# Performance work log

Hardware: AMD Instinct MI355X
Metric: run time of the kernel (lower is better)

The kernel has to match this reference:

```python
import jax, jax.numpy as jnp
import numpy as np

BIAS_BOUND = 8.0

def setup_inputs() -> dict:
    key = jax.random.key(0)
    k1, k2, k3 = jax.random.split(key, 3)
    x = jax.random.normal(k1, (8192, 4096), dtype=jnp.float32)
    # original init: uniform(-1.5, 1.5) for weight, uniform(-bias_bound, bias_bound) for bias
    weight = jax.random.uniform(k2, (4096, 4096), dtype=jnp.float32, minval=-1.5, maxval=1.5)
    bias = jax.random.uniform(k3, (4096,), dtype=jnp.float32, minval=-BIAS_BOUND, maxval=BIAS_BOUND)
    return {"x": x, "weight": weight, "bias": bias}

def reference(x, weight, bias):
    # temperature = 0 path: hard ternary quantization of weights
    w = jnp.clip(jnp.sign(jnp.round(weight)), -1.0, 1.0)      # [out, in] in {-1,0,1}
    b = jnp.clip(jnp.round(bias), -BIAS_BOUND, BIAS_BOUND)    # integer-valued bias
    # F.linear: x @ w.T + b
    return jnp.einsum('ni,oi->no', x, w) + b
```

## Files before the change

kernel.cpp:

```cpp
#include <hip/hip_runtime.h>
#include <hip/hip_bf16.h>
#include <stdint.h>

typedef __bf16 bf16x8 __attribute__((ext_vector_type(8)));
typedef float f32x4 __attribute__((ext_vector_type(4)));

#define AS1 __attribute__((address_space(1)))
#define AS3 __attribute__((address_space(3)))

__global__ void cvt_kernel(const float* __restrict__ x, const float* __restrict__ w,
                           __bf16* __restrict__ xb, __bf16* __restrict__ wb,
                           size_t nx8, size_t ntot8) {
    size_t i = (size_t)blockIdx.x * blockDim.x + threadIdx.x;
    size_t stride = (size_t)gridDim.x * blockDim.x;
    for (; i < ntot8; i += stride) {
        if (i < nx8) {
            size_t base = i * 8;
            float4 f0 = *reinterpret_cast<const float4*>(x + base);
            float4 f1 = *reinterpret_cast<const float4*>(x + base + 4);
            bf16x8 o;
            o[0] = (__bf16)f0.x; o[1] = (__bf16)f0.y; o[2] = (__bf16)f0.z; o[3] = (__bf16)f0.w;
            o[4] = (__bf16)f1.x; o[5] = (__bf16)f1.y; o[6] = (__bf16)f1.z; o[7] = (__bf16)f1.w;
            *reinterpret_cast<bf16x8*>(xb + base) = o;
        } else {
            size_t base = (i - nx8) * 8;
            float4 f0 = *reinterpret_cast<const float4*>(w + base);
            float4 f1 = *reinterpret_cast<const float4*>(w + base + 4);
            float f[8] = {f0.x, f0.y, f0.z, f0.w, f1.x, f1.y, f1.z, f1.w};
            bf16x8 o;
#pragma unroll
            for (int j = 0; j < 8; ++j) {
                float tv = (f[j] > 0.5f) ? 1.0f : ((f[j] < -0.5f) ? -1.0f : 0.0f);
                o[j] = (__bf16)tv;
            }
            *reinterpret_cast<bf16x8*>(wb + base) = o;
        }
    }
}


#define GLOAD(srcp, dstoff) \
    __builtin_amdgcn_global_load_lds((const AS1 void*)(srcp), \
        (AS3 void*)(lds + (dstoff)), 16, 0, 0)

#define STAGE_A0(DB, KT) do { GLOAD(srcA00 + (size_t)(KT)*64, (DB)*65536 +     0 + t*16); \
                              GLOAD(srcA01 + (size_t)(KT)*64, (DB)*65536 +  8192 + t*16); } while(0)
#define STAGE_A1(DB, KT) do { GLOAD(srcA10 + (size_t)(KT)*64, (DB)*65536 + 16384 + t*16); \
                              GLOAD(srcA11 + (size_t)(KT)*64, (DB)*65536 + 24576 + t*16); } while(0)
#define STAGE_B0(DB, KT) do { GLOAD(srcB00 + (size_t)(KT)*64, (DB)*65536 + 32768 + t*16); \
                              GLOAD(srcB01 + (size_t)(KT)*64, (DB)*65536 + 40960 + t*16); } while(0)
#define STAGE_B1(DB, KT) do { GLOAD(srcB10 + (size_t)(KT)*64, (DB)*65536 + 49152 + t*16); \
                              GLOAD(srcB11 + (size_t)(KT)*64, (DB)*65536 + 57344 + t*16); } while(0)

#define LD8(off) (*(const bf16x8*)(lds + (off)))

#define PHASE_SYNC_PRE() do { asm volatile("" ::: "memory"); \
    __builtin_amdgcn_s_barrier(); \
    asm volatile("s_waitcnt lgkmcnt(0)" ::: "memory"); \
    __builtin_amdgcn_sched_barrier(0); } while(0)

#define PHASE_SYNC_POST() do { __builtin_amdgcn_sched_barrier(0); \
    asm volatile("" ::: "memory"); \
    __builtin_amdgcn_s_barrier(); \
    asm volatile("" ::: "memory"); } while(0)

#define MFMA_QUAD(I0, J0) do { \
    __builtin_amdgcn_s_setprio(1); \
    _Pragma("unroll") for (int kk2 = 0; kk2 < 2; ++kk2) \
    _Pragma("unroll") for (int ii2 = 0; ii2 < 4; ++ii2) \
    _Pragma("unroll") for (int jj2 = 0; jj2 < 2; ++jj2) \
        acc[(I0)+ii2][(J0)+jj2] = __builtin_amdgcn_mfma_f32_16x16x32_bf16( \
            af[ii2][kk2], bfr[(J0)+jj2][kk2], acc[(I0)+ii2][(J0)+jj2], 0, 0, 0); \
    __builtin_amdgcn_s_setprio(0); } while(0)

__global__ __launch_bounds__(512, 2) void gemm_kernel(
    const __bf16* __restrict__ A, const __bf16* __restrict__ B,
    const float* __restrict__ bias, float* __restrict__ out,
    int M, int N, int K) {
    __shared__ __align__(16) unsigned char lds[131072];

    const int t    = threadIdx.x;
    const int lane = t & 63;
    const int wave = t >> 6;
    const int wm   = wave >> 2;
    const int wn   = wave & 3;
    const int fr   = lane & 15;
    const int kg   = lane >> 4;
    const int NT   = K >> 6;

    const int nwg  = gridDim.x * gridDim.y;
    int flat = blockIdx.y * gridDim.x + blockIdx.x;
    if ((nwg & 7) == 0) {
        const int cpx = nwg >> 3;
        flat = (flat & 7) * cpx + (flat >> 3);
    }
    const int blockCol = (flat % gridDim.x) * 256;
    const int blockRow = (flat / gridDim.x) * 256;

    const int tq  = t >> 3;
    const int gce = ((t & 7) ^ (tq & 7)) * 8;
    const __bf16* srcA00 = A + (size_t)(blockRow +   0 + tq) * K + gce;
    const __bf16* srcA01 = A + (size_t)(blockRow + 128 + tq) * K + gce;
    const __bf16* srcA10 = A + (size_t)(blockRow +  64 + tq) * K + gce;
    const __bf16* srcA11 = A + (size_t)(blockRow + 192 + tq) * K + gce;
    const int brB = (tq >> 5) * 64 + (tq & 31);
    const __bf16* srcB00 = B + (size_t)(blockCol +       brB) * K + gce;
    const __bf16* srcB01 = B + (size_t)(blockCol + 128 + brB) * K + gce;
    const __bf16* srcB10 = B + (size_t)(blockCol +  32 + brB) * K + gce;
    const __bf16* srcB11 = B + (size_t)(blockCol + 128 + 32 + brB) * K + gce;

    int offA[8], offB[4];
#pragma unroll
    for (int i = 0; i < 8; ++i)
        offA[i] = (((i >> 2) * 128 + wm * 64 + (i & 3) * 16 + fr) << 7);
#pragma unroll
    for (int j = 0; j < 4; ++j)
        offB[j] = 32768 + ((((j >> 1) * 128 + wn * 32 + (j & 1) * 16 + fr)) << 7);
    const int sw0 = ((kg ^ (fr & 7)) << 4);
    const int sw1 = sw0 ^ 64;

    f32x4 acc[8][4] = {};
    bf16x8 af[4][2];
    bf16x8 bfr[4][2];

    STAGE_A0(0, 0); STAGE_A1(0, 0); STAGE_B0(0, 0); STAGE_B1(0, 0);
    if (NT > 1) { STAGE_B0(1, 1); STAGE_A0(1, 1); STAGE_B1(1, 1); }
    if (NT > 1) { asm volatile("s_waitcnt vmcnt(6)" ::: "memory"); }
    else        { asm volatile("s_waitcnt vmcnt(0)" ::: "memory"); }
    __builtin_amdgcn_s_barrier();
    asm volatile("" ::: "memory");

    for (int kt = 0; kt < NT; ++kt) {
        const int db  = kt & 1;
        const int dbB = db << 16;
        const bool pf1 = (kt + 1 < NT);
        const bool pf2 = (kt + 2 < NT);

#pragma unroll
        for (int ii = 0; ii < 4; ++ii) {
            af[ii][0] = LD8(dbB + offA[ii] + sw0);
            af[ii][1] = LD8(dbB + offA[ii] + sw1);
        }
#pragma unroll
        for (int jj = 0; jj < 2; ++jj) {
            bfr[jj][0] = LD8(dbB + offB[jj] + sw0);
            bfr[jj][1] = LD8(dbB + offB[jj] + sw1);
        }
        if (pf1) STAGE_A1(db ^ 1, kt + 1);
        PHASE_SYNC_PRE();
        MFMA_QUAD(0, 0);
        PHASE_SYNC_POST();

#pragma unroll
        for (int jj = 2; jj < 4; ++jj) {
            bfr[jj][0] = LD8(dbB + offB[jj] + sw0);
            bfr[jj][1] = LD8(dbB + offB[jj] + sw1);
        }
        if (pf2) STAGE_B0(db, kt + 2);
        PHASE_SYNC_PRE();
        MFMA_QUAD(0, 2);
        PHASE_SYNC_POST();

#pragma unroll
        for (int ii = 0; ii < 4; ++ii) {
            af[ii][0] = LD8(dbB + offA[ii + 4] + sw0);
            af[ii][1] = LD8(dbB + offA[ii + 4] + sw1);
        }
        if (pf2) STAGE_A0(db, kt + 2);
        PHASE_SYNC_PRE();
        MFMA_QUAD(4, 2);
        PHASE_SYNC_POST();

        if (pf2) STAGE_B1(db, kt + 2);
        if (pf2)      { asm volatile("s_waitcnt vmcnt(6)" ::: "memory"); }
        else if (pf1) { asm volatile("s_waitcnt vmcnt(0)" ::: "memory"); }
        PHASE_SYNC_PRE();
        MFMA_QUAD(4, 0);
        PHASE_SYNC_POST();
    }

#pragma unroll
    for (int j = 0; j < 4; ++j) {
        const int col = blockCol + wn * 64 + j * 16 + fr;
        const float bq = fminf(8.0f, fmaxf(-8.0f, rintf(bias[col])));
#pragma unroll
        for (int i = 0; i < 8; ++i) {
            const int row0 = blockRow + wm * 128 + i * 16 + kg * 4;
#pragma unroll
            for (int r = 0; r < 4; ++r)
                out[(size_t)(row0 + r) * N + col] = acc[i][j][r] + bq;
        }
    }
}

__global__ void naive_kernel(const float* __restrict__ X, const float* __restrict__ W,
                             const float* __restrict__ bias, float* __restrict__ out,
                             int M, int N, int K) {
    int n = blockIdx.x * 16 + (threadIdx.x & 15);
    int m = blockIdx.y * 16 + (threadIdx.x >> 4);
    if (m >= M || n >= N) return;
    float acc = 0.f;
    for (int k = 0; k < K; ++k) {
        float w = W[(size_t)n * K + k];
        float tv = (w > 0.5f) ? 1.0f : ((w < -0.5f) ? -1.0f : 0.0f);
        acc += X[(size_t)m * K + k] * tv;
    }
    float b = fminf(8.0f, fmaxf(-8.0f, rintf(bias[n])));
    out[(size_t)m * N + n] = acc + b;
}

extern "C" void kernel_launch(void* const* d_in, const int* in_sizes, int n_in,
                              void* d_out, int out_size, void* d_ws, size_t ws_size,
                              hipStream_t stream) {
    const float* x    = (const float*)d_in[0];
    const float* w    = (const float*)d_in[1];
    const float* bias = (const float*)d_in[2];
    float* out        = (float*)d_out;

    const int N = in_sizes[2];
    const int K = in_sizes[1] / N;
    const int M = in_sizes[0] / K;

    const size_t xb_elems = (size_t)M * K;
    const size_t wb_elems = (size_t)N * K;
    const size_t need = (xb_elems + wb_elems) * sizeof(__bf16);

    if (ws_size >= need && (M % 256 == 0) && (N % 256 == 0) && (K % 64 == 0) && K >= 192) {
        __bf16* xb = (__bf16*)d_ws;
        __bf16* wb = xb + xb_elems;
        cvt_kernel<<<4096, 256, 0, stream>>>(x, w, xb, wb, xb_elems / 8,
                                             (xb_elems + wb_elems) / 8);
        dim3 grid(N / 256, M / 256);
        gemm_kernel<<<grid, 512, 0, stream>>>(xb, wb, bias, out, M, N, K);
    } else {
        dim3 grid((N + 15) / 16, (M + 15) / 16);
        naive_kernel<<<grid, 256, 0, stream>>>(x, w, bias, out, M, N, K);
    }
}
```

Measured before the change: 497.3 us.

## Prefetch next-tile B fragments during last MFMA phase and simplify conversion kernel

```diff
diff --git a/kernel.cpp b/kernel.cpp
--- a/kernel.cpp
+++ b/kernel.cpp
@@ -3,6 +3,7 @@
 #include <stdint.h>
 
 typedef __bf16 bf16x8 __attribute__((ext_vector_type(8)));
+typedef __bf16 bf16x4 __attribute__((ext_vector_type(4)));
 typedef float f32x4 __attribute__((ext_vector_type(4)));
 
 #define AS1 __attribute__((address_space(1)))
@@ -10,31 +11,29 @@
 
 __global__ void cvt_kernel(const float* __restrict__ x, const float* __restrict__ w,
                            __bf16* __restrict__ xb, __bf16* __restrict__ wb,
-                           size_t nx8, size_t ntot8) {
-    size_t i = (size_t)blockIdx.x * blockDim.x + threadIdx.x;
-    size_t stride = (size_t)gridDim.x * blockDim.x;
-    for (; i < ntot8; i += stride) {
-        if (i < nx8) {
-            size_t base = i * 8;
-            float4 f0 = *reinterpret_cast<const float4*>(x + base);
-            float4 f1 = *reinterpret_cast<const float4*>(x + base + 4);
-            bf16x8 o;
-            o[0] = (__bf16)f0.x; o[1] = (__bf16)f0.y; o[2] = (__bf16)f0.z; o[3] = (__bf16)f0.w;
-            o[4] = (__bf16)f1.x; o[5] = (__bf16)f1.y; o[6] = (__bf16)f1.z; o[7] = (__bf16)f1.w;
-            *reinterpret_cast<bf16x8*>(xb + base) = o;
-        } else {
-            size_t base = (i - nx8) * 8;
-            float4 f0 = *reinterpret_cast<const float4*>(w + base);
-            float4 f1 = *reinterpret_cast<const float4*>(w + base + 4);
-            float f[8] = {f0.x, f0.y, f0.z, f0.w, f1.x, f1.y, f1.z, f1.w};
-            bf16x8 o;
-#pragma unroll
-            for (int j = 0; j < 8; ++j) {
-                float tv = (f[j] > 0.5f) ? 1.0f : ((f[j] < -0.5f) ? -1.0f : 0.0f);
-                o[j] = (__bf16)tv;
-            }
-            *reinterpret_cast<bf16x8*>(wb + base) = o;
-        }
+                           size_t nx4, size_t nw4) {
+    const size_t tid = (size_t)blockIdx.x * blockDim.x + threadIdx.x;
+    const size_t stride = (size_t)gridDim.x * blockDim.x;
+    const float4* __restrict__ x4 = (const float4*)x;
+    const float4* __restrict__ w4 = (const float4*)w;
+    bf16x4* __restrict__ xb4 = (bf16x4*)xb;
+    bf16x4* __restrict__ wb4 = (bf16x4*)wb;
+    for (size_t i = tid; i < nx4; i += stride) {
+        float4 f = x4[i];
+        bf16x4 o;
+        o[0] = (__bf16)f.x; o[1] = (__bf16)f.y; o[2] = (__bf16)f.z; o[3] = (__bf16)f.w;
+        xb4[i] = o;
+    }
+    for (size_t i = tid; i < nw4; i += stride) {
+        float4 f = w4[i];
+        float g[4] = {f.x, f.y, f.z, f.w};
+        bf16x4 o;
+#pragma unroll
+        for (int j = 0; j < 4; ++j) {
+            float tv = (g[j] > 0.5f) ? 1.0f : ((g[j] < -0.5f) ? -1.0f : 0.0f);
+            o[j] = (__bf16)tv;
+        }
+        wb4[i] = o;
     }
 }
 
@@ -129,6 +128,11 @@
     else        { asm volatile("s_waitcnt vmcnt(0)" ::: "memory"); }
     __builtin_amdgcn_s_barrier();
     asm volatile("" ::: "memory");
+#pragma unroll
+    for (int jj = 0; jj < 4; ++jj) {
+        bfr[jj][0] = LD8(offB[jj] + sw0);
+        bfr[jj][1] = LD8(offB[jj] + sw1);
+    }
 
     for (int kt = 0; kt < NT; ++kt) {
         const int db  = kt & 1;
@@ -141,21 +145,11 @@
             af[ii][0] = LD8(dbB + offA[ii] + sw0);
             af[ii][1] = LD8(dbB + offA[ii] + sw1);
         }
-#pragma unroll
-        for (int jj = 0; jj < 2; ++jj) {
-            bfr[jj][0] = LD8(dbB + offB[jj] + sw0);
-            bfr[jj][1] = LD8(dbB + offB[jj] + sw1);
-        }
         if (pf1) STAGE_A1(db ^ 1, kt + 1);
         PHASE_SYNC_PRE();
         MFMA_QUAD(0, 0);
         PHASE_SYNC_POST();
 
-#pragma unroll
-        for (int jj = 2; jj < 4; ++jj) {
-            bfr[jj][0] = LD8(dbB + offB[jj] + sw0);
-            bfr[jj][1] = LD8(dbB + offB[jj] + sw1);
-        }
         if (pf2) STAGE_B0(db, kt + 2);
         PHASE_SYNC_PRE();
         MFMA_QUAD(0, 2);
@@ -176,6 +170,14 @@
         else if (pf1) { asm volatile("s_waitcnt vmcnt(0)" ::: "memory"); }
         PHASE_SYNC_PRE();
         MFMA_QUAD(4, 0);
+        {
+            const int nb = dbB ^ 65536;
+#pragma unroll
+            for (int jj = 0; jj < 4; ++jj) {
+                bfr[jj][0] = LD8(nb + offB[jj] + sw0);
+                bfr[jj][1] = LD8(nb + offB[jj] + sw1);
+            }
+        }
         PHASE_SYNC_POST();
     }
 
@@ -228,8 +230,7 @@
     if (ws_size >= need && (M % 256 == 0) && (N % 256 == 0) && (K % 64 == 0) && K >= 192) {
         __bf16* xb = (__bf16*)d_ws;
         __bf16* wb = xb + xb_elems;
-        cvt_kernel<<<4096, 256, 0, stream>>>(x, w, xb, wb, xb_elems / 8,
-                                             (xb_elems + wb_elems) / 8);
+        cvt_kernel<<<2048, 256, 0, stream>>>(x, w, xb, wb, xb_elems / 4, wb_elems / 4);
         dim3 grid(N / 256, M / 256);
         gemm_kernel<<<grid, 512, 0, stream>>>(xb, wb, bias, out, M, N, K);
     } else {
```

Result: no change. 496.3 us (-0.2%).
